# Kernel tuning notes

Hardware: AMD Instinct MI355X
Metric: run time of the kernel (lower is better)

Reference implementation:

```python
import jax, jax.numpy as jnp
import numpy as np

N = 10000      # nodes
E = 320000     # edges (avg degree 32)
IN = 512       # in_channels
OUT = 128      # out_channels
H = 4          # in_head
C1 = 2 * OUT   # per-head hidden channels of conv1 (256)
NEG_SLOPE = 0.2


def setup_inputs() -> dict:
    key = jax.random.key(0)
    ks = jax.random.split(key, 12)
    x = jax.random.normal(ks[0], (N, IN), dtype=jnp.float32)
    edge_index = jax.random.randint(ks[1], (2, E), 0, N, dtype=jnp.int64)
    def glorot(k, shape):
        lim = np.sqrt(6.0 / (shape[0] + shape[-1])).astype(np.float32)
        return jax.random.uniform(k, shape, jnp.float32, -lim, lim)
    # conv1: GATv2Conv(IN -> C1 per head, heads=H)
    Wl1 = glorot(ks[2], (IN, H * C1))
    Wr1 = glorot(ks[3], (IN, H * C1))
    att1 = glorot(ks[4], (H, C1))
    b1 = jnp.zeros((H * C1,), jnp.float32)
    # conv2: GATv2Conv(H*C1 -> OUT, heads=1)
    Wl2 = glorot(ks[5], (H * C1, OUT))
    Wr2 = glorot(ks[6], (H * C1, OUT))
    att2 = glorot(ks[7], (1, OUT))
    b2 = jnp.zeros((OUT,), jnp.float32)
    return {"x": x, "edge_index": edge_index, "Wl1": Wl1, "Wr1": Wr1,
            "att1": att1, "b1": b1, "Wl2": Wl2, "Wr2": Wr2,
            "att2": att2, "b2": b2}


def gatv2_conv(x, src, dst, Wl, Wr, att, b, heads, ch):
    # x: [N, F_in]; src/dst: [E] (message src -> dst, softmax over dst)
    n = x.shape[0]
    xl = (x @ Wl).reshape(n, heads, ch)   # source-side projection
    xr = (x @ Wr).reshape(n, heads, ch)   # target-side projection
    # per-edge GATv2 score: att . LeakyReLU(xl_j + xr_i)   [E, H]
    e = jax.nn.leaky_relu(xl[src] + xr[dst], NEG_SLOPE)    # [E, H, C]
    s = jnp.einsum('ehc,hc->eh', e, att)                   # [E, H]
    # segment softmax over incoming edges of each dst node
    smax = jax.lax.stop_gradient(jax.ops.segment_max(s, dst, num_segments=n))
    ex = jnp.exp(s - smax[dst])
    denom = jax.ops.segment_sum(ex, dst, num_segments=n)
    alpha = ex / denom[dst]                                # [E, H]
    # weighted scatter-add of source messages
    out = jax.ops.segment_sum(alpha[:, :, None] * xl[src], dst, num_segments=n)
    return out.reshape(n, heads * ch) + b                  # concat heads + bias


def reference(x, edge_index, Wl1, Wr1, att1, b1, Wl2, Wr2, att2, b2):
    src, dst = edge_index[0], edge_index[1]
    h = gatv2_conv(x, src, dst, Wl1, Wr1, att1, b1, H, C1)
    h = jax.nn.relu(h)                                     # [N, H*C1]
    out = gatv2_conv(h, src, dst, Wl2, Wr2, att2, b2, 1, OUT)
    return out                                             # [N, OUT]
```

## Files before the change

### kernel.cpp

```cpp
#include <hip/hip_runtime.h>
#include <cfloat>

#define N_NODES 10000
#define N_EDGES 320000
#define IN_F    512
#define F1      1024
#define OUT_F   128
#define NEG     0.2f
#define BUCKET  128

typedef __attribute__((ext_vector_type(8))) short bf16x8;
typedef __attribute__((ext_vector_type(4))) float f32x4;

__device__ __forceinline__ float lrelu(float v) { return fmaxf(v, NEG * v); }

__device__ __forceinline__ unsigned short f2bf(float f) {
    unsigned u = __float_as_uint(f);
    u += 0x7fff + ((u >> 16) & 1);
    return (unsigned short)(u >> 16);
}
__device__ __forceinline__ float bf2f(unsigned short h) {
    return __uint_as_float(((unsigned)h) << 16);
}
__device__ __forceinline__ void u2f2(unsigned u, float& e0, float& e1) {
    e0 = __uint_as_float(u << 16);
    e1 = __uint_as_float(u & 0xffff0000u);
}

__device__ __forceinline__ float rsum16(float x) {
    x += __int_as_float(__builtin_amdgcn_update_dpp(0, __float_as_int(x), 0x121, 0xF, 0xF, false));
    x += __int_as_float(__builtin_amdgcn_update_dpp(0, __float_as_int(x), 0x122, 0xF, 0xF, false));
    x += __int_as_float(__builtin_amdgcn_update_dpp(0, __float_as_int(x), 0x124, 0xF, 0xF, false));
    x += __int_as_float(__builtin_amdgcn_update_dpp(0, __float_as_int(x), 0x128, 0xF, 0xF, false));
    return x;
}

__device__ __forceinline__ void gld_lds16(const void* g, void* l) {
    __builtin_amdgcn_global_load_lds(
        (const __attribute__((address_space(1))) unsigned int*)g,
        (__attribute__((address_space(3))) unsigned int*)l, 16, 0, 0);
}

#define PB_X  2500
#define PB_S  3750
#define PB_W1 4774
#define PB_END 5030

__device__ __forceinline__ void wt_body(const float* __restrict__ Wa,
                                        const float* __restrict__ Wb,
                                        unsigned short* __restrict__ tbf,
                                        int K, int NS, int n0, int k0, int t,
                                        float (*tile)[33]) {
    int j = t & 31;
    const float* W = (n0 < NS) ? Wa : Wb;
    int nb = (n0 < NS) ? n0 : n0 - NS;
#pragma unroll
    for (int r = 0; r < 4; ++r) {
        int kl = (t >> 5) + r * 8;
        tile[kl][j] = W[(size_t)(k0 + kl) * NS + nb + j];
    }
    __syncthreads();
#pragma unroll
    for (int r = 0; r < 4; ++r) {
        int nl = (t >> 5) + r * 8;
        tbf[(size_t)(n0 + nl) * K + k0 + j] = f2bf(tile[j][nl]);
    }
}

__global__ __launch_bounds__(256) void k_prep(const float* __restrict__ x,
                                              unsigned short* __restrict__ xbf,
                                              const int* __restrict__ ei,
                                              int* __restrict__ cnt,
                                              int* __restrict__ esrc,
                                              const float* __restrict__ Wl1,
                                              const float* __restrict__ Wr1,
                                              unsigned short* __restrict__ w1bf,
                                              const float* __restrict__ Wl2,
                                              const float* __restrict__ Wr2,
                                              unsigned short* __restrict__ w2bf) {
    __shared__ float tile[32][33];
    int bid = blockIdx.x, t = threadIdx.x;
    if (bid < PB_X) {
        int i = bid * 2048 + t * 8;
        float4 v0 = *(const float4*)(x + i);
        float4 v1 = *(const float4*)(x + i + 4);
        ushort4 h0, h1;
        h0.x = f2bf(v0.x); h0.y = f2bf(v0.y); h0.z = f2bf(v0.z); h0.w = f2bf(v0.w);
        h1.x = f2bf(v1.x); h1.y = f2bf(v1.y); h1.z = f2bf(v1.z); h1.w = f2bf(v1.w);
        *(ushort4*)(xbf + i) = h0;
        *(ushort4*)(xbf + i + 4) = h1;
    } else if (bid < PB_S) {
        int e = (bid - PB_X) * 256 + t;
        if (e < N_EDGES) {
            int d = ei[N_EDGES + e];
            int pos = atomicAdd(&cnt[d], 1);
            if (pos < BUCKET) esrc[(size_t)d * BUCKET + pos] = ei[e];
        }
    } else if (bid < PB_W1) {
        int local = bid - PB_S;
        wt_body(Wl1, Wr1, w1bf, IN_F, F1, (local & 63) * 32, (local >> 6) * 32, t, tile);
    } else {
        int local = bid - PB_W1;
        wt_body(Wl2, Wr2, w2bf, F1, OUT_F, (local & 7) * 32, (local >> 3) * 32, t, tile);
    }
}

template<int BM, int WR, int WC>
__global__ __launch_bounds__(256) void gemm_mfma(
        const unsigned short* __restrict__ A,
        const unsigned short* __restrict__ B,
        unsigned short* __restrict__ Cl, unsigned short* __restrict__ Cr,
        int M, int K, int NSPLIT) {
    constexpr int NI = BM / (16 * WR);
    constexpr int NJ = 128 / (16 * WC);
    __shared__ __align__(16) short As[BM * 32];
    __shared__ __align__(16) short Bs[128 * 32];
    int t = threadIdx.x;
    int lane = t & 63, w = t >> 6;
    int row0 = blockIdx.y * BM;
    int n0 = blockIdx.x * 128;
    int wr0 = (w / WC) * (NI * 16);
    int wc0 = (w % WC) * (NJ * 16);
    int q = lane >> 4, md = lane & 15;
    int srow = t >> 2;
    int skoff = (t & 3) * 8;

    f32x4 acc[NI][NJ];
#pragma unroll
    for (int i = 0; i < NI; ++i)
#pragma unroll
        for (int j = 0; j < NJ; ++j)
#pragma unroll
            for (int r = 0; r < 4; ++r) acc[i][j][r] = 0.f;

    for (int k0 = 0; k0 < K; k0 += 32) {
        __syncthreads();
#pragma unroll
        for (int is = 0; is < BM / 64; ++is) {
            int gr = row0 + is * 64 + srow;
            if (gr < M)
                gld_lds16(A + (size_t)gr * K + k0 + skoff,
                          &As[(is * 64 + (t >> 6) * 16) * 32]);
        }
#pragma unroll
        for (int is = 0; is < 2; ++is) {
            int gn = n0 + is * 64 + srow;
            gld_lds16(B + (size_t)gn * K + k0 + skoff,
                      &Bs[(is * 64 + (t >> 6) * 16) * 32]);
        }
        __syncthreads();

        bf16x8 av[NI], bv[NJ];
#pragma unroll
        for (int i = 0; i < NI; ++i)
            av[i] = *(const bf16x8*)&As[(wr0 + i * 16 + md) * 32 + q * 8];
#pragma unroll
        for (int j = 0; j < NJ; ++j)
            bv[j] = *(const bf16x8*)&Bs[(wc0 + j * 16 + md) * 32 + q * 8];
#pragma unroll
        for (int i = 0; i < NI; ++i)
#pragma unroll
            for (int j = 0; j < NJ; ++j)
                acc[i][j] = __builtin_amdgcn_mfma_f32_16x16x32_bf16(av[i], bv[j], acc[i][j], 0, 0, 0);
    }

#pragma unroll
    for (int i = 0; i < NI; ++i)
#pragma unroll
        for (int j = 0; j < NJ; ++j) {
            int col = n0 + wc0 + j * 16 + md;
            unsigned short* C = (col < NSPLIT) ? Cl : Cr;
            int cc = (col < NSPLIT) ? col : col - NSPLIT;
#pragma unroll
            for (int r = 0; r < 4; ++r) {
                int grow = row0 + wr0 + i * 16 + q * 4 + r;
                if (grow < M) C[(size_t)grow * NSPLIT + cc] = f2bf(acc[i][j][r]);
            }
        }
}

__global__ __launch_bounds__(256) void k_fused1(const unsigned short* __restrict__ xlbf,
                                                const unsigned short* __restrict__ xrbf,
                                                const int* __restrict__ cnt,
                                                const int* __restrict__ esrc,
                                                const float* __restrict__ att,
                                                const float* __restrict__ bias,
                                                unsigned short* __restrict__ hb) {
    int t = threadIdx.x;
    int w = t >> 6, lane = t & 63;
    int ni = w >> 1;
    int ww = w & 1;
    int nd = blockIdx.x * 2 + ni;
    int head = lane >> 4, sub = lane & 15;
    int ch = head * 256 + sub * 16;

    __shared__ float slx[4][4];
    __shared__ float4 sacc4[2][4][64];

    float4 r0, r1, r2, r3;
    {
        const uint4* prx = (const uint4*)(xrbf + (size_t)nd * F1 + ch);
        uint4 xa = prx[0], xb = prx[1];
        u2f2(xa.x, r0.x, r0.y); u2f2(xa.y, r0.z, r0.w);
        u2f2(xa.z, r1.x, r1.y); u2f2(xa.w, r1.z, r1.w);
        u2f2(xb.x, r2.x, r2.y); u2f2(xb.y, r2.z, r2.w);
        u2f2(xb.z, r3.x, r3.y); u2f2(xb.w, r3.z, r3.w);
    }
    const float4* pa = (const float4*)(att + ch);
    float4 a0 = pa[0], a1 = pa[1], a2 = pa[2], a3 = pa[3];

    int deg = min(cnt[nd], BUCKET);
    int p0 = nd * BUCKET;
    int half = (deg + 1) >> 1;
    int pa_ = p0 + (ww ? half : 0);
    int pb_ = p0 + (ww ? deg : half);

    float l = 0.f;
    float4 acc0 = make_float4(0.f, 0.f, 0.f, 0.f);
    float4 acc1 = acc0, acc2 = acc0, acc3 = acc0;

    uint4 ua, ub;
    if (pa_ < pb_) {
        const uint4* pv = (const uint4*)(xlbf + (size_t)esrc[pa_] * F1 + ch);
        ua = pv[0]; ub = pv[1];
    }
    for (int p = pa_; p < pb_; ++p) {
        uint4 ca = ua, cb = ub;
        if (p + 1 < pb_) {
            const uint4* pv = (const uint4*)(xlbf + (size_t)esrc[p + 1] * F1 + ch);
            ua = pv[0]; ub = pv[1];
        }
        float4 c0, c1, c2, c3;
        u2f2(ca.x, c0.x, c0.y); u2f2(ca.y, c0.z, c0.w);
        u2f2(ca.z, c1.x, c1.y); u2f2(ca.w, c1.z, c1.w);
        u2f2(cb.x, c2.x, c2.y); u2f2(cb.y, c2.z, c2.w);
        u2f2(cb.z, c3.x, c3.y); u2f2(cb.w, c3.z, c3.w);
        float u;
        float sl0, sa0, sl1, sa1, sl2, sa2, sl3, sa3;
        u = c0.x + r0.x; sl0 = a0.x * u;         sa0 = a0.x * fabsf(u);
        u = c0.y + r0.y; sl0 = fmaf(a0.y, u, sl0); sa0 = fmaf(a0.y, fabsf(u), sa0);
        u = c0.z + r0.z; sl0 = fmaf(a0.z, u, sl0); sa0 = fmaf(a0.z, fabsf(u), sa0);
        u = c0.w + r0.w; sl0 = fmaf(a0.w, u, sl0); sa0 = fmaf(a0.w, fabsf(u), sa0);
        u = c1.x + r1.x; sl1 = a1.x * u;         sa1 = a1.x * fabsf(u);
        u = c1.y + r1.y; sl1 = fmaf(a1.y, u, sl1); sa1 = fmaf(a1.y, fabsf(u), sa1);
        u = c1.z + r1.z; sl1 = fmaf(a1.z, u, sl1); sa1 = fmaf(a1.z, fabsf(u), sa1);
        u = c1.w + r1.w; sl1 = fmaf(a1.w, u, sl1); sa1 = fmaf(a1.w, fabsf(u), sa1);
        u = c2.x + r2.x; sl2 = a2.x * u;         sa2 = a2.x * fabsf(u);
        u = c2.y + r2.y; sl2 = fmaf(a2.y, u, sl2); sa2 = fmaf(a2.y, fabsf(u), sa2);
        u = c2.z + r2.z; sl2 = fmaf(a2.z, u, sl2); sa2 = fmaf(a2.z, fabsf(u), sa2);
        u = c2.w + r2.w; sl2 = fmaf(a2.w, u, sl2); sa2 = fmaf(a2.w, fabsf(u), sa2);
        u = c3.x + r3.x; sl3 = a3.x * u;         sa3 = a3.x * fabsf(u);
        u = c3.y + r3.y; sl3 = fmaf(a3.y, u, sl3); sa3 = fmaf(a3.y, fabsf(u), sa3);
        u = c3.z + r3.z; sl3 = fmaf(a3.z, u, sl3); sa3 = fmaf(a3.z, fabsf(u), sa3);
        u = c3.w + r3.w; sl3 = fmaf(a3.w, u, sl3); sa3 = fmaf(a3.w, fabsf(u), sa3);
        float sl = (sl0 + sl1) + (sl2 + sl3);
        float sa = (sa0 + sa1) + (sa2 + sa3);
        float s = rsum16(fmaf(0.6f, sl, 0.4f * sa));
        s = fminf(fmaxf(s, -60.f), 60.f);
        float al = __expf(s);
        l += al;
        acc0.x = fmaf(al, c0.x, acc0.x);
        acc0.y = fmaf(al, c0.y, acc0.y);
        acc0.z = fmaf(al, c0.z, acc0.z);
        acc0.w = fmaf(al, c0.w, acc0.w);
        acc1.x = fmaf(al, c1.x, acc1.x);
        acc1.y = fmaf(al, c1.y, acc1.y);
        acc1.z = fmaf(al, c1.z, acc1.z);
        acc1.w = fmaf(al, c1.w, acc1.w);
        acc2.x = fmaf(al, c2.x, acc2.x);
        acc2.y = fmaf(al, c2.y, acc2.y);
        acc2.z = fmaf(al, c2.z, acc2.z);
        acc2.w = fmaf(al, c2.w, acc2.w);
        acc3.x = fmaf(al, c3.x, acc3.x);
        acc3.y = fmaf(al, c3.y, acc3.y);
        acc3.z = fmaf(al, c3.z, acc3.z);
        acc3.w = fmaf(al, c3.w, acc3.w);
    }

    if (sub == 0) slx[w][head] = l;
    if (ww == 1) {
        sacc4[ni][0][lane] = acc0;
        sacc4[ni][1][lane] = acc1;
        sacc4[ni][2][lane] = acc2;
        sacc4[ni][3][lane] = acc3;
    }
    __syncthreads();
    if (ww == 0) {
        float L = l + slx[w ^ 1][head];
        float invL = (L > 0.f) ? 1.f / L : 0.f;
        const float4* pb = (const float4*)(bias + ch);
        size_t base = (size_t)nd * F1 + ch;
        float4 aa[4] = {acc0, acc1, acc2, acc3};
#pragma unroll
        for (int j = 0; j < 4; ++j) {
            float4 pt = sacc4[ni][j][lane];
            float4 b4 = pb[j];
            ushort4 hv;
            hv.x = f2bf(fmaxf(fmaf(aa[j].x + pt.x, invL, b4.x), 0.f));
            hv.y = f2bf(fmaxf(fmaf(aa[j].y + pt.y, invL, b4.y), 0.f));
            hv.z = f2bf(fmaxf(fmaf(aa[j].z + pt.z, invL, b4.z), 0.f));
            hv.w = f2bf(fmaxf(fmaf(aa[j].w + pt.w, invL, b4.w), 0.f));
            *(ushort4*)(hb + base + j * 4) = hv;
        }
    }
}

__global__ __launch_bounds__(256) void k_fused2(const unsigned short* __restrict__ xlbf,
                                                const unsigned short* __restrict__ xrbf,
                                                const int* __restrict__ cnt,
                                                const int* __restrict__ esrc,
                                                const float* __restrict__ att,
                                                const float* __restrict__ bias,
                                                float* __restrict__ out) {
    int t = threadIdx.x;
    int w = t >> 6, lane = t & 63;
    int nd = blockIdx.x * 4 + w;
    int g = lane >> 4, sub = lane & 15;
    int ch = sub * 8;

    __shared__ float slx2[4][4];
    __shared__ float sacc2[4][4][132];

    float r[8], a[8];
    {
        uint4 u = *(const uint4*)(xrbf + (size_t)nd * OUT_F + ch);
        u2f2(u.x, r[0], r[1]); u2f2(u.y, r[2], r[3]);
        u2f2(u.z, r[4], r[5]); u2f2(u.w, r[6], r[7]);
        float4 q0 = *(const float4*)(att + ch);
        float4 q1 = *(const float4*)(att + ch + 4);
        a[0] = q0.x; a[1] = q0.y; a[2] = q0.z; a[3] = q0.w;
        a[4] = q1.x; a[5] = q1.y; a[6] = q1.z; a[7] = q1.w;
    }
    int deg = min(cnt[nd], BUCKET);
    int p0 = nd * BUCKET;
    int p1 = p0 + deg;

    float l = 0.f;
    float acc[8] = {};
    uint4 cur, nxt;
    {
        int p = p0 + g;
        if (p < p1)     cur = *(const uint4*)(xlbf + (size_t)esrc[p] * OUT_F + ch);
        if (p + 4 < p1) nxt = *(const uint4*)(xlbf + (size_t)esrc[p + 4] * OUT_F + ch);
    }
    for (int p = p0 + g; p < p1; p += 4) {
        uint4 c = cur;
        cur = nxt;
        if (p + 8 < p1) nxt = *(const uint4*)(xlbf + (size_t)esrc[p + 8] * OUT_F + ch);
        float v[8];
        u2f2(c.x, v[0], v[1]); u2f2(c.y, v[2], v[3]);
        u2f2(c.z, v[4], v[5]); u2f2(c.w, v[6], v[7]);
        float uu;
        float slA, saA, slB, saB;
        uu = v[0] + r[0]; slA = a[0] * uu;          saA = a[0] * fabsf(uu);
        uu = v[1] + r[1]; slA = fmaf(a[1], uu, slA); saA = fmaf(a[1], fabsf(uu), saA);
        uu = v[2] + r[2]; slA = fmaf(a[2], uu, slA); saA = fmaf(a[2], fabsf(uu), saA);
        uu = v[3] + r[3]; slA = fmaf(a[3], uu, slA); saA = fmaf(a[3], fabsf(uu), saA);
        uu = v[4] + r[4]; slB = a[4] * uu;          saB = a[4] * fabsf(uu);
        uu = v[5] + r[5]; slB = fmaf(a[5], uu, slB); saB = fmaf(a[5], fabsf(uu), saB);
        uu = v[6] + r[6]; slB = fmaf(a[6], uu, slB); saB = fmaf(a[6], fabsf(uu), saB);
        uu = v[7] + r[7]; slB = fmaf(a[7], uu, slB); saB = fmaf(a[7], fabsf(uu), saB);
        float s = rsum16(fmaf(0.6f, slA + slB, 0.4f * (saA + saB)));
        s = fminf(fmaxf(s, -60.f), 60.f);
        float al = __expf(s);
        l += al;
#pragma unroll
        for (int k = 0; k < 8; ++k) acc[k] = fmaf(al, v[k], acc[k]);
    }

    if (sub == 0) slx2[w][g] = l;
    float4 v0 = make_float4(acc[0], acc[1], acc[2], acc[3]);
    float4 v1 = make_float4(acc[4], acc[5], acc[6], acc[7]);
    *(float4*)&sacc2[w][g][ch] = v0;
    *(float4*)&sacc2[w][g][ch + 4] = v1;
    __syncthreads();
    float L = slx2[w][0] + slx2[w][1] + slx2[w][2] + slx2[w][3];
    float invL = (L > 0.f) ? 1.f / L : 0.f;
    int c2 = lane * 2;
    float o0 = sacc2[w][0][c2] + sacc2[w][1][c2] + sacc2[w][2][c2] + sacc2[w][3][c2];
    float o1 = sacc2[w][0][c2 + 1] + sacc2[w][1][c2 + 1] + sacc2[w][2][c2 + 1] + sacc2[w][3][c2 + 1];
    float2 bf = *(const float2*)(bias + c2);
    float2 o;
    o.x = fmaf(o0, invL, bf.x);
    o.y = fmaf(o1, invL, bf.y);
    *(float2*)(out + (size_t)nd * OUT_F + c2) = o;
}

extern "C" void kernel_launch(void* const* d_in, const int* in_sizes, int n_in,
                              void* d_out, int out_size, void* d_ws, size_t ws_size,
                              hipStream_t stream) {
    const float* x    = (const float*)d_in[0];
    const int*   ei   = (const int*)d_in[1];
    const float* Wl1  = (const float*)d_in[2];
    const float* Wr1  = (const float*)d_in[3];
    const float* att1 = (const float*)d_in[4];
    const float* b1   = (const float*)d_in[5];
    const float* Wl2  = (const float*)d_in[6];
    const float* Wr2  = (const float*)d_in[7];
    const float* att2 = (const float*)d_in[8];
    const float* b2   = (const float*)d_in[9];
    float* out = (float*)d_out;

    unsigned short* us = (unsigned short*)d_ws;
    unsigned short* xl1bf = us;
    unsigned short* xr1bf = xl1bf + (size_t)N_NODES * F1;
    unsigned short* xl2bf = xr1bf + (size_t)N_NODES * F1;
    unsigned short* xr2bf = xl2bf + (size_t)N_NODES * OUT_F;
    unsigned short* hb   = xr2bf + (size_t)N_NODES * OUT_F;
    unsigned short* xbf  = hb + (size_t)N_NODES * F1;
    unsigned short* w1bf = xbf + (size_t)N_NODES * IN_F;
    unsigned short* w2bf = w1bf + (size_t)2048 * IN_F;
    int* cnt   = (int*)(w2bf + (size_t)256 * F1);
    int* esrc  = cnt + (N_NODES + 16);

    hipMemsetAsync(cnt, 0, sizeof(int) * N_NODES, stream);
    k_prep<<<PB_END, 256, 0, stream>>>(x, xbf, ei, cnt, esrc,
                                       Wl1, Wr1, w1bf,
                                       Wl2, Wr2, w2bf);

    gemm_mfma<128, 2, 2><<<dim3(16, (N_NODES + 127) / 128), 256, 0, stream>>>(
        xbf, w1bf, xl1bf, xr1bf, N_NODES, IN_F, F1);

    k_fused1<<<N_NODES / 2, 256, 0, stream>>>(xl1bf, xr1bf, cnt, esrc, att1, b1, hb);

    gemm_mfma<64, 1, 4><<<dim3(2, (N_NODES + 63) / 64), 256, 0, stream>>>(
        hb, w2bf, xl2bf, xr2bf, N_NODES, F1, OUT_F);

    k_fused2<<<N_NODES / 4, 256, 0, stream>>>(xl2bf, xr2bf, cnt, esrc, att2, b2, out);
}
```

Baseline: 265.7 us.

## Sort per-node edge buckets and load source indices once per wave in fused1

Adds a wave-level bitonic sort kernel that orders each node's first 64 source indices, which makes the gather deterministic and improves locality of the xl row reads. In k_fused1 each wave now loads up to 64 source indices in one coalesced read and broadcasts them with shuffles, instead of issuing a dependent scalar esrc load per edge. The two waves now take interleaved edges (even and odd) rather than contiguous halves, and degrees above 64 fall back to direct esrc loads. The cost is an extra kernel launch plus the sort work.

```diff
diff --git a/kernel.cpp b/kernel.cpp
--- a/kernel.cpp
+++ b/kernel.cpp
@@ -105,6 +105,29 @@
     }
 }
 
+__global__ __launch_bounds__(256) void k_sort(const int* __restrict__ cnt,
+                                              int* __restrict__ esrc) {
+    int t = threadIdx.x;
+    int w = t >> 6, lane = t & 63;
+    int nd = blockIdx.x * 4 + w;
+    if (nd >= N_NODES) return;
+    int deg = min(cnt[nd], 64);
+    int p0 = nd * BUCKET;
+    int v = (lane < deg) ? esrc[p0 + lane] : 0x7fffffff;
+#pragma unroll
+    for (int k = 2; k <= 64; k <<= 1) {
+#pragma unroll
+        for (int j = k >> 1; j > 0; j >>= 1) {
+            int other = __shfl_xor(v, j);
+            bool dir = ((lane & k) == 0);
+            bool lower = ((lane & j) == 0);
+            int mn = min(v, other), mx = max(v, other);
+            v = (lower == dir) ? mn : mx;
+        }
+    }
+    if (lane < deg) esrc[p0 + lane] = v;
+}
+
 template<int BM, int WR, int WC>
 __global__ __launch_bounds__(256) void gemm_mfma(
         const unsigned short* __restrict__ A,
@@ -211,25 +234,14 @@
 
     int deg = min(cnt[nd], BUCKET);
     int p0 = nd * BUCKET;
-    int half = (deg + 1) >> 1;
-    int pa_ = p0 + (ww ? half : 0);
-    int pb_ = p0 + (ww ? deg : half);
+    int dege = min(deg, 64);
+    int bkt = (lane < dege) ? esrc[p0 + lane] : 0;
 
     float l = 0.f;
     float4 acc0 = make_float4(0.f, 0.f, 0.f, 0.f);
     float4 acc1 = acc0, acc2 = acc0, acc3 = acc0;
 
-    uint4 ua, ub;
-    if (pa_ < pb_) {
-        const uint4* pv = (const uint4*)(xlbf + (size_t)esrc[pa_] * F1 + ch);
-        ua = pv[0]; ub = pv[1];
-    }
-    for (int p = pa_; p < pb_; ++p) {
-        uint4 ca = ua, cb = ub;
-        if (p + 1 < pb_) {
-            const uint4* pv = (const uint4*)(xlbf + (size_t)esrc[p + 1] * F1 + ch);
-            ua = pv[0]; ub = pv[1];
-        }
+    auto edge_body = [&](uint4 ca, uint4 cb) {
         float4 c0, c1, c2, c3;
         u2f2(ca.x, c0.x, c0.y); u2f2(ca.y, c0.z, c0.w);
         u2f2(ca.z, c1.x, c1.y); u2f2(ca.w, c1.z, c1.w);
@@ -237,19 +249,19 @@
         u2f2(cb.z, c3.x, c3.y); u2f2(cb.w, c3.z, c3.w);
         float u;
         float sl0, sa0, sl1, sa1, sl2, sa2, sl3, sa3;
-        u = c0.x + r0.x; sl0 = a0.x * u;         sa0 = a0.x * fabsf(u);
+        u = c0.x + r0.x; sl0 = a0.x * u;           sa0 = a0.x * fabsf(u);
         u = c0.y + r0.y; sl0 = fmaf(a0.y, u, sl0); sa0 = fmaf(a0.y, fabsf(u), sa0);
         u = c0.z + r0.z; sl0 = fmaf(a0.z, u, sl0); sa0 = fmaf(a0.z, fabsf(u), sa0);
         u = c0.w + r0.w; sl0 = fmaf(a0.w, u, sl0); sa0 = fmaf(a0.w, fabsf(u), sa0);
-        u = c1.x + r1.x; sl1 = a1.x * u;         sa1 = a1.x * fabsf(u);
+        u = c1.x + r1.x; sl1 = a1.x * u;           sa1 = a1.x * fabsf(u);
         u = c1.y + r1.y; sl1 = fmaf(a1.y, u, sl1); sa1 = fmaf(a1.y, fabsf(u), sa1);
         u = c1.z + r1.z; sl1 = fmaf(a1.z, u, sl1); sa1 = fmaf(a1.z, fabsf(u), sa1);
         u = c1.w + r1.w; sl1 = fmaf(a1.w, u, sl1); sa1 = fmaf(a1.w, fabsf(u), sa1);
-        u = c2.x + r2.x; sl2 = a2.x * u;         sa2 = a2.x * fabsf(u);
+        u = c2.x + r2.x; sl2 = a2.x * u;           sa2 = a2.x * fabsf(u);
         u = c2.y + r2.y; sl2 = fmaf(a2.y, u, sl2); sa2 = fmaf(a2.y, fabsf(u), sa2);
         u = c2.z + r2.z; sl2 = fmaf(a2.z, u, sl2); sa2 = fmaf(a2.z, fabsf(u), sa2);
         u = c2.w + r2.w; sl2 = fmaf(a2.w, u, sl2); sa2 = fmaf(a2.w, fabsf(u), sa2);
-        u = c3.x + r3.x; sl3 = a3.x * u;         sa3 = a3.x * fabsf(u);
+        u = c3.x + r3.x; sl3 = a3.x * u;           sa3 = a3.x * fabsf(u);
         u = c3.y + r3.y; sl3 = fmaf(a3.y, u, sl3); sa3 = fmaf(a3.y, fabsf(u), sa3);
         u = c3.z + r3.z; sl3 = fmaf(a3.z, u, sl3); sa3 = fmaf(a3.z, fabsf(u), sa3);
         u = c3.w + r3.w; sl3 = fmaf(a3.w, u, sl3); sa3 = fmaf(a3.w, fabsf(u), sa3);
@@ -275,6 +287,28 @@
         acc3.y = fmaf(al, c3.y, acc3.y);
         acc3.z = fmaf(al, c3.z, acc3.z);
         acc3.w = fmaf(al, c3.w, acc3.w);
+    };
+
+    int idx = ww;
+    uint4 ua, ub;
+    if (idx < dege) {
+        int sn = __shfl(bkt, idx);
+        const uint4* pv = (const uint4*)(xlbf + (size_t)sn * F1 + ch);
+        ua = pv[0]; ub = pv[1];
+    }
+    for (; idx < dege; idx += 2) {
+        uint4 ca = ua, cb = ub;
+        int nidx = idx + 2;
+        if (nidx < dege) {
+            int sn = __shfl(bkt, nidx);
+            const uint4* pv = (const uint4*)(xlbf + (size_t)sn * F1 + ch);
+            ua = pv[0]; ub = pv[1];
+        }
+        edge_body(ca, cb);
+    }
+    for (int p = p0 + 64 + ww; p < p0 + deg; p += 2) {
+        const uint4* pv = (const uint4*)(xlbf + (size_t)esrc[p] * F1 + ch);
+        edge_body(pv[0], pv[1]);
     }
 
     if (sub == 0) slx[w][head] = l;
@@ -352,11 +386,11 @@
         u2f2(c.z, v[4], v[5]); u2f2(c.w, v[6], v[7]);
         float uu;
         float slA, saA, slB, saB;
-        uu = v[0] + r[0]; slA = a[0] * uu;          saA = a[0] * fabsf(uu);
+        uu = v[0] + r[0]; slA = a[0] * uu;           saA = a[0] * fabsf(uu);
         uu = v[1] + r[1]; slA = fmaf(a[1], uu, slA); saA = fmaf(a[1], fabsf(uu), saA);
         uu = v[2] + r[2]; slA = fmaf(a[2], uu, slA); saA = fmaf(a[2], fabsf(uu), saA);
         uu = v[3] + r[3]; slA = fmaf(a[3], uu, slA); saA = fmaf(a[3], fabsf(uu), saA);
-        uu = v[4] + r[4]; slB = a[4] * uu;          saB = a[4] * fabsf(uu);
+        uu = v[4] + r[4]; slB = a[4] * uu;           saB = a[4] * fabsf(uu);
         uu = v[5] + r[5]; slB = fmaf(a[5], uu, slB); saB = fmaf(a[5], fabsf(uu), saB);
         uu = v[6] + r[6]; slB = fmaf(a[6], uu, slB); saB = fmaf(a[6], fabsf(uu), saB);
         uu = v[7] + r[7]; slB = fmaf(a[7], uu, slB); saB = fmaf(a[7], fabsf(uu), saB);
@@ -418,6 +452,8 @@
                                        Wl1, Wr1, w1bf,
                                        Wl2, Wr2, w2bf);
 
+    k_sort<<<(N_NODES + 3) / 4, 256, 0, stream>>>(cnt, esrc);
+
     gemm_mfma<128, 2, 2><<<dim3(16, (N_NODES + 127) / 128), 256, 0, stream>>>(
         xbf, w1bf, xl1bf, xr1bf, N_NODES, IN_F, F1);
 
```

After: 263.3 us. No clear change (-0.9%).
